# Performance work log

Measured on AMD Instinct MI355X. Metric: run time of the kernel, lower is better.

Reference implementation:

```python
import jax, jax.numpy as jnp
from jax import lax
import numpy as np

INPUT, HIDDEN, OUTPUT, SEQ, BS = 512, 2048, 512, 4096, 1


def setup_inputs() -> dict:
    key = jax.random.key(0)
    ks = jax.random.split(key, 10)
    s = 0.02
    return {
        "x": jax.random.normal(ks[0], (BS, SEQ, INPUT), jnp.float32),
        "hidden": jax.random.normal(ks[1], (BS, HIDDEN), jnp.float32),
        "Wi": jax.random.normal(ks[2], (HIDDEN, INPUT + HIDDEN), jnp.float32) * s,
        "bi": jnp.zeros((HIDDEN,), jnp.float32),
        "Wg": jax.random.normal(ks[3], (HIDDEN, INPUT + HIDDEN), jnp.float32) * s,
        "bg": jnp.zeros((HIDDEN,), jnp.float32),
        "Wo": jax.random.normal(ks[4], (HIDDEN, INPUT + HIDDEN), jnp.float32) * s,
        "bo": jnp.zeros((HIDDEN,), jnp.float32),
        "Wout": jax.random.normal(ks[5], (OUTPUT, HIDDEN), jnp.float32) * s,
        "bout": jnp.zeros((OUTPUT,), jnp.float32),
    }


def reference(x, hidden, Wi, bi, Wg, bg, Wo, bo, Wout, bout):
    bs = x.shape[0]
    h0 = jnp.zeros((bs, Wi.shape[0]), x.dtype)

    def step(h, xt):
        comb = jnp.concatenate([xt, h], axis=1)  # [bs, in+hid]
        i_t = jax.nn.sigmoid(comb @ Wi.T + bi)
        g_t = jnp.tanh(comb @ Wg.T + bg)
        o_t = jax.nn.sigmoid(comb @ Wo.T + bo)
        # NOTE: no forget gate, no c_{t-1}: c_t = i_t * g_t exactly per source
        h_new = o_t * jnp.tanh(i_t * g_t)
        return h_new, None

    xs = jnp.swapaxes(x, 0, 1)  # [T, bs, in]
    hT, _ = lax.scan(step, h0, xs)
    output = hT @ Wout.T + bout  # last-step output only, per source
    return (output, hidden)
```

## Files before the change

### kernel.cpp

```cpp
#include <hip/hip_runtime.h>
#include <hip/hip_fp16.h>
#include <hip/hip_cooperative_groups.h>

namespace cg = cooperative_groups;

#define T_SEQ 4096
#define D_IN  512
#define D_H   2048
#define D_C   2560
#define D_OUT 512
#define NBLK  256
#define NTHR  512
#define UPB   8
#define SPIN_CAP 4096

typedef unsigned int u32;
typedef u32 u32x4 __attribute__((ext_vector_type(4)));

__device__ __forceinline__ void dot4(float& acc, const float4& a, const float4& b) {
    acc = fmaf(a.x, b.x, acc);
    acc = fmaf(a.y, b.y, acc);
    acc = fmaf(a.z, b.z, acc);
    acc = fmaf(a.w, b.w, acc);
}

template<int CTRL, int RMASK>
__device__ __forceinline__ float dpp_add(float x) {
    int t = __builtin_amdgcn_update_dpp(0, __float_as_int(x), CTRL, RMASK, 0xf, true);
    return x + __int_as_float(t);
}
__device__ __forceinline__ float wave_red63(float x) {
    x = dpp_add<0x111, 0xf>(x);
    x = dpp_add<0x112, 0xf>(x);
    x = dpp_add<0x114, 0xf>(x);
    x = dpp_add<0x118, 0xf>(x);
    x = dpp_add<0x142, 0xa>(x);
    x = dpp_add<0x143, 0xc>(x);
    return x;
}

__device__ __forceinline__ float fast_sigmoid(float z) {
    float e = __builtin_amdgcn_exp2f(-1.44269504f * z);
    return __builtin_amdgcn_rcpf(1.0f + e);
}
__device__ __forceinline__ float fast_tanh(float z) {
    float e2 = __builtin_amdgcn_exp2f(2.88539008f * z);
    return 1.0f - 2.0f * __builtin_amdgcn_rcpf(e2 + 1.0f);
}

#define AW(i, v) asm volatile("v_accvgpr_write_b32 %0, %1" : "=a"(aw[i]) : "v"(v))
#define AR(d, i) asm volatile("v_accvgpr_read_b32 %0, %1" : "=v"(d) : "a"(aw[i]))
#define DOT4A(acc, base, hv) do { float4 _w;                          \
        AR(_w.x, (base) + 0); AR(_w.y, (base) + 1);                   \
        AR(_w.z, (base) + 2); AR(_w.w, (base) + 3);                   \
        dot4(acc, _w, hv); } while (0)

__device__ __forceinline__ u32x4 load_quad_l3(const u32* p) {
    u32x4 v;
    asm volatile("global_load_dwordx4 %0, %1, off sc0 sc1\n\ts_waitcnt vmcnt(0)"
                 : "=&v"(v) : "v"(p) : "memory");
    return v;
}
__device__ __forceinline__ u32x4 load_quad_l2(const u32* p) {
    u32x4 v;
    asm volatile("global_load_dwordx4 %0, %1, off sc0\n\ts_waitcnt vmcnt(0)"
                 : "=&v"(v) : "v"(p) : "memory");
    return v;
}
__device__ __forceinline__ void store_quad_l2(u32* p, u32x4 v) {
    asm volatile("global_store_dwordx4 %0, %1, off" :: "v"(p), "v"(v) : "memory");
}
__device__ __forceinline__ bool tags_ok(u32x4 v, u32 tg) {
    return (v.x >> 16) == tg && (v.y >> 16) == tg &&
           (v.z >> 16) == tg && (v.w >> 16) == tg;
}
__device__ __forceinline__ float4 unpackq(u32x4 v) {
    return make_float4(
        __half2float(__ushort_as_half((unsigned short)(v.x & 0xFFFFu))),
        __half2float(__ushort_as_half((unsigned short)(v.y & 0xFFFFu))),
        __half2float(__ushort_as_half((unsigned short)(v.z & 0xFFFFu))),
        __half2float(__ushort_as_half((unsigned short)(v.w & 0xFFFFu))));
}

__global__ __launch_bounds__(NTHR, 2) void lstm_persist(
    const float* __restrict__ x,
    const float* __restrict__ hidden_in,
    const float* __restrict__ Wi, const float* __restrict__ bi,
    const float* __restrict__ Wg, const float* __restrict__ bg,
    const float* __restrict__ Wo, const float* __restrict__ bo,
    const float* __restrict__ Wout, const float* __restrict__ bout,
    float* __restrict__ out,
    u32* __restrict__ ws)
{
    cg::grid_group grid = cg::this_grid();
    const int tid  = threadIdx.x;
    const int lane = tid & 63;
    const int w    = tid >> 6;
    const int j    = blockIdx.x * UPB + w;
    const int kb   = lane * 4;

    u32* hb2    = ws;
    u32* mirror = ws + 2 * D_H;
    u32* claims = ws + 2 * D_H + 16 * D_H;

    __shared__ float lds_h[D_H];
    __shared__ u32 s_relay;

    if (blockIdx.x == 0) {
        for (int i = tid; i < 2 * D_H + 16 * D_H + 8; i += NTHR)
            __hip_atomic_store(&ws[i], 0u, __ATOMIC_RELAXED, __HIP_MEMORY_SCOPE_AGENT);
    }

    float aw[96];
    float4 wxi0, wxi1, wxg0, wxg1, wxo0, wxo1;
    {
        const size_t rh = (size_t)j * D_C + 512 + kb;
#pragma unroll
        for (int r = 0; r < 8; ++r) {
            const float4 vi = *(const float4*)(Wi + rh + 256 * r);
            const float4 vg = *(const float4*)(Wg + rh + 256 * r);
            const float4 vo = *(const float4*)(Wo + rh + 256 * r);
            AW(r * 4 + 0, vi.x); AW(r * 4 + 1, vi.y);
            AW(r * 4 + 2, vi.z); AW(r * 4 + 3, vi.w);
            AW(32 + r * 4 + 0, vg.x); AW(32 + r * 4 + 1, vg.y);
            AW(32 + r * 4 + 2, vg.z); AW(32 + r * 4 + 3, vg.w);
            AW(64 + r * 4 + 0, vo.x); AW(64 + r * 4 + 1, vo.y);
            AW(64 + r * 4 + 2, vo.z); AW(64 + r * 4 + 3, vo.w);
        }
        const size_t ro = (size_t)j * D_C + kb;
        wxi0 = *(const float4*)(Wi + ro); wxi1 = *(const float4*)(Wi + ro + 256);
        wxg0 = *(const float4*)(Wg + ro); wxg1 = *(const float4*)(Wg + ro + 256);
        wxo0 = *(const float4*)(Wo + ro); wxo1 = *(const float4*)(Wo + ro + 256);
    }
    const float b_i = bi[j];
    const float b_g = bg[j];
    const float b_o = bo[j];

    grid.sync();

    unsigned xcd;
    asm volatile("s_getreg_b32 %0, hwreg(HW_REG_XCC_ID)" : "=s"(xcd));
    xcd &= 7u;
    if (tid == 0) {
        u32 r = __hip_atomic_fetch_add(&claims[xcd], 1u,
                                       __ATOMIC_RELAXED, __HIP_MEMORY_SCOPE_AGENT);
        s_relay = (r == 0u) ? 1u : 0u;
    }
    __syncthreads();
    const bool isRelay = (s_relay != 0u);

    float4 xv0 = *(const float4*)(x + kb);
    float4 xv1 = *(const float4*)(x + kb + 256);

    int use_l2 = 1;

#pragma unroll 1
    for (int t = 0; t < T_SEQ; ++t) {
        float ai = 0.f, ag = 0.f, ao = 0.f;
        dot4(ai, wxi0, xv0); dot4(ai, wxi1, xv1);
        dot4(ag, wxg0, xv0); dot4(ag, wxg1, xv1);
        dot4(ao, wxo0, xv0); dot4(ao, wxo1, xv1);
        const int tn = (t + 1 < T_SEQ) ? t + 1 : t;
        const float4 xn0 = *(const float4*)(x + (size_t)tn * D_IN + kb);
        const float4 xn1 = *(const float4*)(x + (size_t)tn * D_IN + kb + 256);

        const u32 tg = (u32)t & 0xFFFFu;
        const u32* gp = hb2 + (t & 1) * D_H + tid * 4;
        u32x4 v;
        if (isRelay) {
            u32* mp = mirror + ((size_t)xcd * 2 + (t & 1)) * D_H + tid * 4;
            for (;;) { v = load_quad_l3(gp); if (tags_ok(v, tg)) break; }
            store_quad_l2(mp, v);
        } else {
            const u32* mp = mirror + ((size_t)xcd * 2 + (t & 1)) * D_H + tid * 4;
            bool got = false;
            if (use_l2) {
                for (int s = 0; s < SPIN_CAP; ++s) {
                    v = load_quad_l2(mp);
                    if (tags_ok(v, tg)) { got = true; break; }
                }
                if (!got) use_l2 = 0;
            }
            if (!got) {
                for (;;) { v = load_quad_l3(gp); if (tags_ok(v, tg)) break; }
            }
        }
        *(float4*)(&lds_h[tid * 4]) = unpackq(v);
        __syncthreads();

#pragma unroll
        for (int r = 0; r < 8; ++r) {
            const float4 hv = *(const float4*)(&lds_h[r * 256 + kb]);
            DOT4A(ai, r * 4, hv);
            DOT4A(ag, 32 + r * 4, hv);
            DOT4A(ao, 64 + r * 4, hv);
        }

        ai = wave_red63(ai); ag = wave_red63(ag); ao = wave_red63(ao);

        if (lane == 63) {
            const float zi = ai + b_i;
            const float zg = ag + b_g;
            const float zo = ao + b_o;
            const float it = fast_sigmoid(zi);
            const float gt = fast_tanh(zg);
            const float ot = fast_sigmoid(zo);
            const float h  = ot * fast_tanh(it * gt);
            const u32 pk = ((u32)((t + 1) & 0xFFFF) << 16) |
                           (u32)__half_as_ushort(__float2half(h));
            __hip_atomic_store(&hb2[((t + 1) & 1) * D_H + j], pk,
                               __ATOMIC_RELAXED, __HIP_MEMORY_SCOPE_AGENT);
        }
        xv0 = xn0; xv1 = xn1;
    }

    if (isRelay) {
        const u32 tg = (u32)T_SEQ & 0xFFFFu;
        const u32* gp = hb2 + tid * 4;
        u32* mp = mirror + ((size_t)xcd * 2) * D_H + tid * 4;
        u32x4 v;
        for (;;) { v = load_quad_l3(gp); if (tags_ok(v, tg)) break; }
        store_quad_l2(mp, v);
    }

    if (blockIdx.x < 64) {
        const u32 tg = (u32)T_SEQ & 0xFFFFu;
        const u32* gp = hb2 + tid * 4;
        const u32* mp = mirror + ((size_t)xcd * 2) * D_H + tid * 4;
        u32x4 v;
        bool got = false;
        if (use_l2) {
            for (int s = 0; s < SPIN_CAP; ++s) {
                v = load_quad_l2(mp);
                if (tags_ok(v, tg)) { got = true; break; }
            }
        }
        if (!got) {
            for (;;) { v = load_quad_l3(gp); if (tags_ok(v, tg)) break; }
        }
        *(float4*)(&lds_h[tid * 4]) = unpackq(v);
        __syncthreads();

        const int ow = blockIdx.x * 8 + w;
        const float* pw = Wout + (size_t)ow * D_H + kb;
        float acc = 0.f;
#pragma unroll
        for (int r = 0; r < 8; ++r) {
            const float4 w4 = *(const float4*)(pw + 256 * r);
            const float4 hv = *(const float4*)(&lds_h[kb + 256 * r]);
            dot4(acc, w4, hv);
        }
        acc = wave_red63(acc);
        if (lane == 63) out[ow] = acc + bout[ow];
    } else if (blockIdx.x >= 64 && blockIdx.x < 66) {
        const int base = (blockIdx.x - 64) * 1024;
        out[D_OUT + base + tid]       = hidden_in[base + tid];
        out[D_OUT + base + tid + 512] = hidden_in[base + tid + 512];
    }
}

extern "C" void kernel_launch(void* const* d_in, const int* in_sizes, int n_in,
                              void* d_out, int out_size, void* d_ws, size_t ws_size,
                              hipStream_t stream) {
    const float* x      = (const float*)d_in[0];
    const float* hidden = (const float*)d_in[1];
    const float* Wi     = (const float*)d_in[2];
    const float* bi     = (const float*)d_in[3];
    const float* Wg     = (const float*)d_in[4];
    const float* bg     = (const float*)d_in[5];
    const float* Wo     = (const float*)d_in[6];
    const float* bo     = (const float*)d_in[7];
    const float* Wout   = (const float*)d_in[8];
    const float* bout   = (const float*)d_in[9];
    float* out = (float*)d_out;
    u32* ws = (u32*)d_ws;

    void* args[] = {(void*)&x, (void*)&hidden, (void*)&Wi, (void*)&bi,
                    (void*)&Wg, (void*)&bg, (void*)&Wo, (void*)&bo,
                    (void*)&Wout, (void*)&bout, (void*)&out, (void*)&ws};
    (void)hipLaunchCooperativeKernel((const void*)lstm_persist,
                                     dim3(NBLK), dim3(NTHR), args, 0, stream);
}
```

Before: 9.432 ms.

## Dedicate eight relay blocks and redistribute hidden units with ninth-unit split

Reserves the last 8 blocks as dedicated relay blocks that copy each step's h from the global buffer into per-XCD mirrors, instead of using a compute block as relay. The 2048 hidden units are respread over the remaining 248 blocks: 64 blocks take a ninth unit, computed cooperatively across all 8 waves, with its weights reloaded each step and a shared-memory reduction. The intent is to take relay latency off the compute critical path. In exchange the 9-unit blocks do extra per-step global loads, an extra __syncthreads and a cross-wave reduction. The code also assumes each XCD gets exactly one relay block.

New measurement: 20.96 ms. 2.22x slower.

```diff
diff --git a/kernel.cpp b/kernel.cpp
--- a/kernel.cpp
+++ b/kernel.cpp
@@ -10,8 +10,8 @@
 #define D_C   2560
 #define D_OUT 512
 #define NBLK  256
+#define NCOMP 248
 #define NTHR  512
-#define UPB   8
 #define SPIN_CAP 4096
 
 typedef unsigned int u32;
@@ -80,6 +80,9 @@
         __half2float(__ushort_as_half((unsigned short)(v.y & 0xFFFFu))),
         __half2float(__ushort_as_half((unsigned short)(v.z & 0xFFFFu))),
         __half2float(__ushort_as_half((unsigned short)(v.w & 0xFFFFu))));
+}
+__device__ __forceinline__ u32 packh(int tag, float h) {
+    return ((u32)(tag & 0xFFFF) << 16) | (u32)__half_as_ushort(__float2half(h));
 }
 
 __global__ __launch_bounds__(NTHR, 2) void lstm_persist(
@@ -93,23 +96,46 @@
     u32* __restrict__ ws)
 {
     cg::grid_group grid = cg::this_grid();
+    const int b    = blockIdx.x;
     const int tid  = threadIdx.x;
     const int lane = tid & 63;
     const int w    = tid >> 6;
-    const int j    = blockIdx.x * UPB + w;
     const int kb   = lane * 4;
 
     u32* hb2    = ws;
     u32* mirror = ws + 2 * D_H;
-    u32* claims = ws + 2 * D_H + 16 * D_H;
 
     __shared__ float lds_h[D_H];
-    __shared__ u32 s_relay;
-
-    if (blockIdx.x == 0) {
-        for (int i = tid; i < 2 * D_H + 16 * D_H + 8; i += NTHR)
+    __shared__ float part9[3][8];
+
+    if (b == 0) {
+        for (int i = tid; i < 2 * D_H + 16 * D_H; i += NTHR)
             __hip_atomic_store(&ws[i], 0u, __ATOMIC_RELAXED, __HIP_MEMORY_SCOPE_AGENT);
     }
+    grid.sync();
+
+    unsigned xcd;
+    asm volatile("s_getreg_b32 %0, hwreg(HW_REG_XCC_ID)" : "=s"(xcd));
+    xcd &= 7u;
+
+    if (b >= NCOMP) {
+        u32* mpb = mirror + (size_t)xcd * 2 * D_H;
+#pragma unroll 1
+        for (int t = 1; t <= T_SEQ; ++t) {
+            const u32 tg = (u32)t & 0xFFFFu;
+            const u32* gp = hb2 + (t & 1) * D_H + tid * 4;
+            u32*       mp = mpb + (t & 1) * D_H + tid * 4;
+            u32x4 v;
+            for (;;) { v = load_quad_l3(gp); if (tags_ok(v, tg)) break; }
+            store_quad_l2(mp, v);
+        }
+        return;
+    }
+
+    const bool nb9 = (b < 64);
+    const int  ub  = nb9 ? b * 9 : 576 + (b - 64) * 8;
+    const int  j   = ub + w;
+    const int  j9  = ub + 8;
 
     float aw[96];
     float4 wxi0, wxi1, wxg0, wxg1, wxo0, wxo1;
@@ -135,19 +161,8 @@
     const float b_i = bi[j];
     const float b_g = bg[j];
     const float b_o = bo[j];
-
-    grid.sync();
-
-    unsigned xcd;
-    asm volatile("s_getreg_b32 %0, hwreg(HW_REG_XCC_ID)" : "=s"(xcd));
-    xcd &= 7u;
-    if (tid == 0) {
-        u32 r = __hip_atomic_fetch_add(&claims[xcd], 1u,
-                                       __ATOMIC_RELAXED, __HIP_MEMORY_SCOPE_AGENT);
-        s_relay = (r == 0u) ? 1u : 0u;
-    }
-    __syncthreads();
-    const bool isRelay = (s_relay != 0u);
+    float b9i = 0.f, b9g = 0.f, b9o = 0.f;
+    if (nb9) { b9i = bi[j9]; b9g = bg[j9]; b9o = bo[j9]; }
 
     float4 xv0 = *(const float4*)(x + kb);
     float4 xv1 = *(const float4*)(x + kb + 256);
@@ -164,26 +179,33 @@
         const float4 xn0 = *(const float4*)(x + (size_t)tn * D_IN + kb);
         const float4 xn1 = *(const float4*)(x + (size_t)tn * D_IN + kb + 256);
 
+        float4 w9i, w9g, w9o, x9i0, x9i1, x9g0, x9g1, x9o0, x9o1;
+        if (nb9) {
+            const size_t r9 = (size_t)j9 * D_C;
+            w9i = *(const float4*)(Wi + r9 + 512 + w * 256 + kb);
+            w9g = *(const float4*)(Wg + r9 + 512 + w * 256 + kb);
+            w9o = *(const float4*)(Wo + r9 + 512 + w * 256 + kb);
+            if (w == 0) {
+                x9i0 = *(const float4*)(Wi + r9 + kb); x9i1 = *(const float4*)(Wi + r9 + kb + 256);
+                x9g0 = *(const float4*)(Wg + r9 + kb); x9g1 = *(const float4*)(Wg + r9 + kb + 256);
+                x9o0 = *(const float4*)(Wo + r9 + kb); x9o1 = *(const float4*)(Wo + r9 + kb + 256);
+            }
+        }
+
         const u32 tg = (u32)t & 0xFFFFu;
         const u32* gp = hb2 + (t & 1) * D_H + tid * 4;
+        const u32* mp = mirror + ((size_t)xcd * 2 + (t & 1)) * D_H + tid * 4;
         u32x4 v;
-        if (isRelay) {
-            u32* mp = mirror + ((size_t)xcd * 2 + (t & 1)) * D_H + tid * 4;
+        bool got = false;
+        if (use_l2) {
+            for (int s = 0; s < SPIN_CAP; ++s) {
+                v = load_quad_l2(mp);
+                if (tags_ok(v, tg)) { got = true; break; }
+            }
+            if (!got) use_l2 = 0;
+        }
+        if (!got) {
             for (;;) { v = load_quad_l3(gp); if (tags_ok(v, tg)) break; }
-            store_quad_l2(mp, v);
-        } else {
-            const u32* mp = mirror + ((size_t)xcd * 2 + (t & 1)) * D_H + tid * 4;
-            bool got = false;
-            if (use_l2) {
-                for (int s = 0; s < SPIN_CAP; ++s) {
-                    v = load_quad_l2(mp);
-                    if (tags_ok(v, tg)) { got = true; break; }
-                }
-                if (!got) use_l2 = 0;
-            }
-            if (!got) {
-                for (;;) { v = load_quad_l3(gp); if (tags_ok(v, tg)) break; }
-            }
         }
         *(float4*)(&lds_h[tid * 4]) = unpackq(v);
         __syncthreads();
@@ -206,24 +228,44 @@
             const float gt = fast_tanh(zg);
             const float ot = fast_sigmoid(zo);
             const float h  = ot * fast_tanh(it * gt);
-            const u32 pk = ((u32)((t + 1) & 0xFFFF) << 16) |
-                           (u32)__half_as_ushort(__float2half(h));
-            __hip_atomic_store(&hb2[((t + 1) & 1) * D_H + j], pk,
+            __hip_atomic_store(&hb2[((t + 1) & 1) * D_H + j], packh(t + 1, h),
                                __ATOMIC_RELAXED, __HIP_MEMORY_SCOPE_AGENT);
         }
+
+        if (nb9) {
+            float p9i = 0.f, p9g = 0.f, p9o = 0.f;
+            const float4 hv = *(const float4*)(&lds_h[w * 256 + kb]);
+            dot4(p9i, w9i, hv); dot4(p9g, w9g, hv); dot4(p9o, w9o, hv);
+            if (w == 0) {
+                dot4(p9i, x9i0, xv0); dot4(p9i, x9i1, xv1);
+                dot4(p9g, x9g0, xv0); dot4(p9g, x9g1, xv1);
+                dot4(p9o, x9o0, xv0); dot4(p9o, x9o1, xv1);
+            }
+            p9i = wave_red63(p9i); p9g = wave_red63(p9g); p9o = wave_red63(p9o);
+            if (lane == 63) { part9[0][w] = p9i; part9[1][w] = p9g; part9[2][w] = p9o; }
+            __syncthreads();
+            if (w == 0) {
+                float pv = (lane < 24) ? part9[lane >> 3][lane & 7] : 0.f;
+                pv += __shfl_xor(pv, 1, 64);
+                pv += __shfl_xor(pv, 2, 64);
+                pv += __shfl_xor(pv, 4, 64);
+                const float zi = __shfl(pv, 0, 64)  + b9i;
+                const float zg = __shfl(pv, 8, 64)  + b9g;
+                const float zo = __shfl(pv, 16, 64) + b9o;
+                const float it = fast_sigmoid(zi);
+                const float gt = fast_tanh(zg);
+                const float ot = fast_sigmoid(zo);
+                const float h  = ot * fast_tanh(it * gt);
+                if (lane == 0)
+                    __hip_atomic_store(&hb2[((t + 1) & 1) * D_H + j9], packh(t + 1, h),
+                                       __ATOMIC_RELAXED, __HIP_MEMORY_SCOPE_AGENT);
+            }
+        }
+
         xv0 = xn0; xv1 = xn1;
     }
 
-    if (isRelay) {
-        const u32 tg = (u32)T_SEQ & 0xFFFFu;
-        const u32* gp = hb2 + tid * 4;
-        u32* mp = mirror + ((size_t)xcd * 2) * D_H + tid * 4;
-        u32x4 v;
-        for (;;) { v = load_quad_l3(gp); if (tags_ok(v, tg)) break; }
-        store_quad_l2(mp, v);
-    }
-
-    if (blockIdx.x < 64) {
+    if (b < 64) {
         const u32 tg = (u32)T_SEQ & 0xFFFFu;
         const u32* gp = hb2 + tid * 4;
         const u32* mp = mirror + ((size_t)xcd * 2) * D_H + tid * 4;
@@ -241,7 +283,7 @@
         *(float4*)(&lds_h[tid * 4]) = unpackq(v);
         __syncthreads();
 
-        const int ow = blockIdx.x * 8 + w;
+        const int ow = b * 8 + w;
         const float* pw = Wout + (size_t)ow * D_H + kb;
         float acc = 0.f;
 #pragma unroll
@@ -252,8 +294,8 @@
         }
         acc = wave_red63(acc);
         if (lane == 63) out[ow] = acc + bout[ow];
-    } else if (blockIdx.x >= 64 && blockIdx.x < 66) {
-        const int base = (blockIdx.x - 64) * 1024;
+    } else if (b >= 64 && b < 66) {
+        const int base = (b - 64) * 1024;
         out[D_OUT + base + tid]       = hidden_in[base + tid];
         out[D_OUT + base + tid + 512] = hidden_in[base + tid + 512];
     }
```
